# Optimization experiments

Measured on AMD Instinct MI355X. Metric: run time of the kernel, lower is better.

The kernel has to match this reference:

```python
import jax, jax.numpy as jnp
import numpy as np

GROUPS = 32
EPS = 1e-5


def group_norm(x, w, b):
    B, C, H, W = x.shape
    xg = x.reshape(B, GROUPS, C // GROUPS, H, W)
    mu = xg.mean(axis=(2, 3, 4), keepdims=True)
    var = xg.var(axis=(2, 3, 4), keepdims=True)
    xn = ((xg - mu) / jnp.sqrt(var + EPS)).reshape(B, C, H, W)
    return xn * w[None, :, None, None] + b[None, :, None, None]


def setup_inputs() -> dict:
    key = jax.random.key(0)
    ks = jax.random.split(key, 4)
    B, C, H, W = 8, 512, 32, 32
    x = jax.random.normal(ks[0], (B, C, H, W), dtype=jnp.float32)
    gn_w = jnp.ones((C,), dtype=jnp.float32)
    gn_b = jnp.zeros((C,), dtype=jnp.float32)
    # 1x1 conv weights, scaled like typical init for numerical sanity
    qkv_w = jax.random.normal(ks[1], (3 * C, C), dtype=jnp.float32) * (1.0 / np.sqrt(C))
    proj_w = jax.random.normal(ks[2], (C, C), dtype=jnp.float32) * (1.0 / np.sqrt(C))
    proj_b = jnp.zeros((C,), dtype=jnp.float32)
    return {"x": x, "gn_w": gn_w, "gn_b": gn_b, "qkv_w": qkv_w,
            "proj_w": proj_w, "proj_b": proj_b, "num_heads": 8}


def reference(x, gn_w, gn_b, qkv_w, proj_w, proj_b, num_heads):
    B, C, H, W = x.shape
    N = H * W
    head_dim = C // num_heads
    xn = group_norm(x, gn_w, gn_b)
    # 1x1 conv == channel matmul: (B, 3C, N)
    qkv = jnp.einsum('oc,bcn->bon', qkv_w, xn.reshape(B, C, N))
    # faithful to torch: reshape to (B*nh, 3*hd, N) then chunk into thirds
    qkv = qkv.reshape(B * num_heads, 3 * head_dim, N)
    q, k, v = jnp.split(qkv, 3, axis=1)  # each (B*nh, hd, N)
    scale = 1.0 / np.sqrt(np.sqrt(head_dim))
    attn = jax.nn.softmax(jnp.einsum('bct,bcs->bts', q * scale, k * scale), axis=-1)
    h = jnp.einsum('bts,bcs->bct', attn, v)  # (B*nh, hd, N)
    h = h.reshape(B, C, N)
    out = jnp.einsum('oc,bcn->bon', proj_w, h) + proj_b[None, :, None]
    return out.reshape(B, C, H, W) + x
```

## Files before the change

### kernel.cpp

```cpp
#include <hip/hip_runtime.h>

#define B_ 8
#define C_ 512
#define N_ 1024
#define GROUPS_ 32
#define CPG_ 16
#define NH_ 8
#define HD_ 64

typedef _Float16 half8 __attribute__((ext_vector_type(8)));
typedef float f32x4 __attribute__((ext_vector_type(4)));

__global__ __launch_bounds__(256) void cvt_kernel(const float* __restrict__ in,
                                                  _Float16* __restrict__ out,
                                                  int n) {
  const int i = (blockIdx.x * 256 + threadIdx.x) * 4;
  if (i < n) {
    const float4 v = *reinterpret_cast<const float4*>(&in[i]);
    _Float16 h[4] = {(_Float16)v.x, (_Float16)v.y, (_Float16)v.z, (_Float16)v.w};
    *reinterpret_cast<uint2*>(&out[i]) = *reinterpret_cast<uint2*>(&h[0]);
  }
}

__global__ __launch_bounds__(256) void gn_kernel(const float* __restrict__ x,
                                                 const float* __restrict__ gw,
                                                 const float* __restrict__ gb,
                                                 _Float16* __restrict__ xnT) {
  const int bg = blockIdx.x;
  const int b = bg / GROUPS_, g = bg % GROUPS_;
  const float* xp = x + ((size_t)b * C_ + (size_t)g * CPG_) * N_;
  const int tid = threadIdx.x;
  const int total = CPG_ * N_;

  float s = 0.f, ss = 0.f;
  for (int i = tid * 4; i < total; i += 1024) {
    const float4 v = *reinterpret_cast<const float4*>(xp + i);
    s += v.x + v.y + v.z + v.w;
    ss += v.x * v.x + v.y * v.y + v.z * v.z + v.w * v.w;
  }
#pragma unroll
  for (int off = 32; off > 0; off >>= 1) {
    s += __shfl_down(s, off);
    ss += __shfl_down(ss, off);
  }
  __shared__ float red[8];
  __shared__ float stat[2];
  if ((tid & 63) == 0) { red[tid >> 6] = s; red[4 + (tid >> 6)] = ss; }
  __syncthreads();
  if (tid == 0) {
    s = red[0] + red[1] + red[2] + red[3];
    ss = red[4] + red[5] + red[6] + red[7];
    const float inv = 1.0f / (float)total;
    const float mu = s * inv;
    const float var = ss * inv - mu * mu;
    stat[0] = mu;
    stat[1] = rsqrtf(var + 1e-5f);
  }
  __syncthreads();
  __shared__ float wsh[CPG_], bsh[CPG_];
  if (tid < CPG_) {
    const float w = gw[g * CPG_ + tid] * stat[1];
    wsh[tid] = w;
    bsh[tid] = gb[g * CPG_ + tid] - stat[0] * w;
  }
  __syncthreads();
#pragma unroll
  for (int it = 0; it < 4; ++it) {
    const int n = it * 256 + tid;
    _Float16 h[CPG_];
#pragma unroll
    for (int c = 0; c < CPG_; ++c)
      h[c] = (_Float16)(xp[c * N_ + n] * wsh[c] + bsh[c]);
    _Float16* dst = &xnT[((size_t)b * N_ + n) * C_ + g * CPG_];
    *reinterpret_cast<uint4*>(dst) = *reinterpret_cast<uint4*>(&h[0]);
    *reinterpret_cast<uint4*>(dst + 8) = *reinterpret_cast<uint4*>(&h[8]);
  }
}

template <bool OUT_HALF, bool EPI>
__global__ __launch_bounds__(256) void gemm_tn(
    const _Float16* __restrict__ A, long strideAb,
    const _Float16* __restrict__ Bm, long strideBb,
    void* __restrict__ D, long strideDb, int ldd, int K,
    const float* __restrict__ bias, const float* __restrict__ resid,
    long strideRb) {
  const int bc0 = blockIdx.x * 128;
  const int ar0 = blockIdx.y * 128;
  const int b = blockIdx.z;
  const _Float16* Ab = A + (size_t)b * strideAb;
  const _Float16* Bb = Bm + (size_t)b * strideBb;

  __shared__ _Float16 As[128][40];
  __shared__ _Float16 Bs[128][40];

  const int tid = threadIdx.x;
  const int lane = tid & 63;
  const int wid = tid >> 6;
  const int war = (wid >> 1) * 64;
  const int wbc = (wid & 1) * 64;
  const int lg = lane >> 4;
  const int lr = lane & 15;

  const int srow = tid >> 1;
  const int skoff = (tid & 1) * 16;

  f32x4 acc[4][4] = {};

  for (int k0 = 0; k0 < K; k0 += 32) {
    __syncthreads();
    const float4 av0 = *reinterpret_cast<const float4*>(
        &Ab[(size_t)(ar0 + srow) * K + k0 + skoff]);
    const float4 av1 = *reinterpret_cast<const float4*>(
        &Ab[(size_t)(ar0 + srow) * K + k0 + skoff + 8]);
    const float4 bv0 = *reinterpret_cast<const float4*>(
        &Bb[(size_t)(bc0 + srow) * K + k0 + skoff]);
    const float4 bv1 = *reinterpret_cast<const float4*>(
        &Bb[(size_t)(bc0 + srow) * K + k0 + skoff + 8]);
    *reinterpret_cast<float4*>(&As[srow][skoff]) = av0;
    *reinterpret_cast<float4*>(&As[srow][skoff + 8]) = av1;
    *reinterpret_cast<float4*>(&Bs[srow][skoff]) = bv0;
    *reinterpret_cast<float4*>(&Bs[srow][skoff + 8]) = bv1;
    __syncthreads();

    half8 af[4], bf[4];
#pragma unroll
    for (int i = 0; i < 4; ++i)
      af[i] = *reinterpret_cast<const half8*>(&As[war + i * 16 + lr][lg * 8]);
#pragma unroll
    for (int j = 0; j < 4; ++j)
      bf[j] = *reinterpret_cast<const half8*>(&Bs[wbc + j * 16 + lr][lg * 8]);
#pragma unroll
    for (int i = 0; i < 4; ++i)
#pragma unroll
      for (int j = 0; j < 4; ++j)
        acc[i][j] = __builtin_amdgcn_mfma_f32_16x16x32_f16(af[i], bf[j],
                                                           acc[i][j], 0, 0, 0);
  }

  if (OUT_HALF) {
    _Float16* Dp = (_Float16*)D + (size_t)b * strideDb;
#pragma unroll
    for (int i = 0; i < 4; ++i)
#pragma unroll
      for (int r = 0; r < 4; ++r) {
        const int row = ar0 + war + i * 16 + lg * 4 + r;
#pragma unroll
        for (int j = 0; j < 4; ++j) {
          const int col = bc0 + wbc + j * 16 + lr;
          Dp[(size_t)row * ldd + col] = (_Float16)acc[i][j][r];
        }
      }
  }
  if (EPI) {
    float* Dp = (float*)D + (size_t)b * strideDb;
    const float* Rp = resid + (size_t)b * strideRb;
#pragma unroll
    for (int i = 0; i < 4; ++i)
#pragma unroll
      for (int r = 0; r < 4; ++r) {
        const int row = ar0 + war + i * 16 + lg * 4 + r;
        const float bv = bias[row];
#pragma unroll
        for (int j = 0; j < 4; ++j) {
          const int col = bc0 + wbc + j * 16 + lr;
          const size_t off = (size_t)row * ldd + col;
          Dp[off] = acc[i][j][r] + bv + Rp[off];
        }
      }
  }
}

__global__ __launch_bounds__(256) void attn_mfma(const _Float16* __restrict__ qkvT,
                                                 _Float16* __restrict__ hT) {
  const int qt = blockIdx.x;
  const int bh = blockIdx.y;
  const int b = bh >> 3, head = bh & 7;
  const int qb = qt * 64;
  const size_t base = (size_t)b * N_ * 1536 + head * 192;

  __shared__ _Float16 Qs[64][72];
  __shared__ _Float16 Ks[64][72];
  __shared__ _Float16 Vs[64][72];
  __shared__ _Float16 Ps[64][72];

  const int tid = threadIdx.x;
  const int lane = tid & 63;
  const int wid = tid >> 6;
  const int lg = lane >> 4, lr = lane & 15;
  const int tw = wid * 16;
  const int ss = tid >> 2;
  const int sc = (tid & 3) * 16;

  {
    const _Float16* qp = &qkvT[base + (size_t)(qb + ss) * 1536 + sc];
    *reinterpret_cast<float4*>(&Qs[ss][sc]) =
        *reinterpret_cast<const float4*>(qp);
    *reinterpret_cast<float4*>(&Qs[ss][sc + 8]) =
        *reinterpret_cast<const float4*>(qp + 8);
  }

  f32x4 oacc[4] = {};
  float m_run[4], l_run[4];
#pragma unroll
  for (int r = 0; r < 4; ++r) { m_run[r] = -1e30f; l_run[r] = 0.f; }

  for (int sb = 0; sb < N_; sb += 64) {
    __syncthreads();
    {
      const _Float16* kp = &qkvT[base + 64 + (size_t)(sb + ss) * 1536 + sc];
      *reinterpret_cast<float4*>(&Ks[ss][sc]) =
          *reinterpret_cast<const float4*>(kp);
      *reinterpret_cast<float4*>(&Ks[ss][sc + 8]) =
          *reinterpret_cast<const float4*>(kp + 8);
      const _Float16* vp = &qkvT[base + 128 + (size_t)(sb + ss) * 1536 + sc];
      const float4 v0 = *reinterpret_cast<const float4*>(vp);
      const float4 v1 = *reinterpret_cast<const float4*>(vp + 8);
      const _Float16* vh0 = reinterpret_cast<const _Float16*>(&v0);
      const _Float16* vh1 = reinterpret_cast<const _Float16*>(&v1);
#pragma unroll
      for (int ii = 0; ii < 8; ++ii) Vs[sc + ii][ss] = vh0[ii];
#pragma unroll
      for (int ii = 0; ii < 8; ++ii) Vs[sc + 8 + ii][ss] = vh1[ii];
    }
    __syncthreads();

    const half8 qa0 = *reinterpret_cast<const half8*>(&Qs[tw + lr][lg * 8]);
    const half8 qa1 = *reinterpret_cast<const half8*>(&Qs[tw + lr][32 + lg * 8]);
    f32x4 sacc[4] = {};
#pragma unroll
    for (int j = 0; j < 4; ++j) {
      const half8 kb0 = *reinterpret_cast<const half8*>(&Ks[j * 16 + lr][lg * 8]);
      const half8 kb1 =
          *reinterpret_cast<const half8*>(&Ks[j * 16 + lr][32 + lg * 8]);
      sacc[j] = __builtin_amdgcn_mfma_f32_16x16x32_f16(qa0, kb0, sacc[j], 0, 0, 0);
      sacc[j] = __builtin_amdgcn_mfma_f32_16x16x32_f16(qa1, kb1, sacc[j], 0, 0, 0);
    }

#pragma unroll
    for (int r = 0; r < 4; ++r) {
      float mt = -1e30f;
#pragma unroll
      for (int j = 0; j < 4; ++j) {
        sacc[j][r] *= 0.125f;
        mt = fmaxf(mt, sacc[j][r]);
      }
      mt = fmaxf(mt, __shfl_xor(mt, 1));
      mt = fmaxf(mt, __shfl_xor(mt, 2));
      mt = fmaxf(mt, __shfl_xor(mt, 4));
      mt = fmaxf(mt, __shfl_xor(mt, 8));
      const float mn = fmaxf(m_run[r], mt);
      const float alpha = __expf(m_run[r] - mn);
      m_run[r] = mn;
      float ps = 0.f;
#pragma unroll
      for (int j = 0; j < 4; ++j) {
        const float p = __expf(sacc[j][r] - mn);
        sacc[j][r] = p;
        ps += p;
      }
      ps += __shfl_xor(ps, 1);
      ps += __shfl_xor(ps, 2);
      ps += __shfl_xor(ps, 4);
      ps += __shfl_xor(ps, 8);
      l_run[r] = l_run[r] * alpha + ps;
#pragma unroll
      for (int j = 0; j < 4; ++j) {
        oacc[j][r] *= alpha;
        Ps[tw + lg * 4 + r][j * 16 + lr] = (_Float16)sacc[j][r];
      }
    }

    const half8 pa0 = *reinterpret_cast<const half8*>(&Ps[tw + lr][lg * 8]);
    const half8 pa1 = *reinterpret_cast<const half8*>(&Ps[tw + lr][32 + lg * 8]);
#pragma unroll
    for (int j = 0; j < 4; ++j) {
      const half8 vb0 = *reinterpret_cast<const half8*>(&Vs[j * 16 + lr][lg * 8]);
      const half8 vb1 =
          *reinterpret_cast<const half8*>(&Vs[j * 16 + lr][32 + lg * 8]);
      oacc[j] = __builtin_amdgcn_mfma_f32_16x16x32_f16(pa0, vb0, oacc[j], 0, 0, 0);
      oacc[j] = __builtin_amdgcn_mfma_f32_16x16x32_f16(pa1, vb1, oacc[j], 0, 0, 0);
    }
  }

  const size_t hbase = (size_t)b * N_ * C_ + head * HD_;
#pragma unroll
  for (int r = 0; r < 4; ++r) {
    const float inv = 1.f / l_run[r];
    const int t = tw + lg * 4 + r;
#pragma unroll
    for (int j = 0; j < 4; ++j)
      hT[hbase + (size_t)(qb + t) * C_ + j * 16 + lr] =
          (_Float16)(oacc[j][r] * inv);
  }
}

extern "C" void kernel_launch(void* const* d_in, const int* in_sizes, int n_in,
                              void* d_out, int out_size, void* d_ws,
                              size_t ws_size, hipStream_t stream) {
  const float* x = (const float*)d_in[0];
  const float* gn_w = (const float*)d_in[1];
  const float* gn_b = (const float*)d_in[2];
  const float* qkv_w = (const float*)d_in[3];
  const float* proj_w = (const float*)d_in[4];
  const float* proj_b = (const float*)d_in[5];
  float* out = (float*)d_out;

  char* ws = (char*)d_ws;
  _Float16* qw_h = (_Float16*)ws;
  _Float16* pw_h = (_Float16*)(ws + (size_t)1572864);
  _Float16* xnT = (_Float16*)(ws + (size_t)2 * 1024 * 1024);
  _Float16* qkvT = (_Float16*)(ws + (size_t)10 * 1024 * 1024);
  _Float16* hT = (_Float16*)(ws + (size_t)34 * 1024 * 1024);

  cvt_kernel<<<dim3(768), 256, 0, stream>>>(qkv_w, qw_h, 3 * C_ * C_);
  cvt_kernel<<<dim3(256), 256, 0, stream>>>(proj_w, pw_h, C_ * C_);
  gn_kernel<<<dim3(B_ * GROUPS_), 256, 0, stream>>>(x, gn_w, gn_b, xnT);
  gemm_tn<true, false><<<dim3(12, 8, B_), 256, 0, stream>>>(
      xnT, (long)N_ * C_, qw_h, 0L, qkvT, (long)N_ * 3 * C_, 3 * C_, C_,
      nullptr, nullptr, 0L);
  attn_mfma<<<dim3(N_ / 64, B_ * NH_), 256, 0, stream>>>(qkvT, hT);
  gemm_tn<false, true><<<dim3(8, 4, B_), 256, 0, stream>>>(
      pw_h, 0L, hT, (long)N_ * C_, out, (long)C_ * N_, N_, C_,
      proj_b, x, (long)C_ * N_);
}
```

Measured before the change: 209.2 us.

## Restructure attention with 32x32 MFMA, register Q, prefetch, and V-transposed GEMM

Weights are packed into separate QK and V matrices, with the Q rows pre-scaled by the softmax scale times log2(e). V is then produced by its own GEMM directly in transposed layout, which removes the scattered LDS transpose inside attention. Group norm is split into a stats kernel and a normalize kernel that transposes through shared memory for coalesced stores. Attention now uses 32x32x16 MFMA with 256 queries per block and Q held in registers, and it prefetches the next K/V tile into registers. Softmax uses exp2 and skips the rescale unless the max grows past a threshold, and P is kept in registers via lane shuffles instead of LDS. The risks are higher register pressure, lower occupancy with 256 blocks, and fp16 overflow from the lazy rescale.

```diff
diff --git a/kernel.cpp b/kernel.cpp
--- a/kernel.cpp
+++ b/kernel.cpp
@@ -9,23 +9,47 @@
 #define HD_ 64
 
 typedef _Float16 half8 __attribute__((ext_vector_type(8)));
+typedef _Float16 half2v __attribute__((ext_vector_type(2)));
 typedef float f32x4 __attribute__((ext_vector_type(4)));
-
-__global__ __launch_bounds__(256) void cvt_kernel(const float* __restrict__ in,
-                                                  _Float16* __restrict__ out,
-                                                  int n) {
-  const int i = (blockIdx.x * 256 + threadIdx.x) * 4;
-  if (i < n) {
-    const float4 v = *reinterpret_cast<const float4*>(&in[i]);
-    _Float16 h[4] = {(_Float16)v.x, (_Float16)v.y, (_Float16)v.z, (_Float16)v.w};
-    *reinterpret_cast<uint2*>(&out[i]) = *reinterpret_cast<uint2*>(&h[0]);
-  }
-}
-
-__global__ __launch_bounds__(256) void gn_kernel(const float* __restrict__ x,
-                                                 const float* __restrict__ gw,
-                                                 const float* __restrict__ gb,
-                                                 _Float16* __restrict__ xnT) {
+typedef float f32x16 __attribute__((ext_vector_type(16)));
+
+#define QSCALE 0.18033688011112042f
+#define THR_LOG2 11.0f
+
+__global__ __launch_bounds__(256) void pack_weights(
+    const float* __restrict__ qkv_w, const float* __restrict__ proj_w,
+    _Float16* __restrict__ qkw, _Float16* __restrict__ vw,
+    _Float16* __restrict__ pw) {
+  const int R = blockIdx.x * 4 + (threadIdx.x >> 6);
+  const int k = (threadIdx.x & 63) * 8;
+  const float* src;
+  _Float16* dst;
+  float sc = 1.f;
+  if (R < 1024) {
+    const int head = R >> 7, r = R & 127;
+    src = qkv_w + (size_t)(head * 192 + r) * 512;
+    if (r < 64) sc = QSCALE;
+    dst = qkw + (size_t)R * 512;
+  } else if (R < 1536) {
+    const int vr = R - 1024;
+    const int head = vr >> 6, c = vr & 63;
+    src = qkv_w + (size_t)(head * 192 + 128 + c) * 512;
+    dst = vw + (size_t)vr * 512;
+  } else {
+    src = proj_w + (size_t)(R - 1536) * 512;
+    dst = pw + (size_t)(R - 1536) * 512;
+  }
+  const float4 v0 = *reinterpret_cast<const float4*>(src + k);
+  const float4 v1 = *reinterpret_cast<const float4*>(src + k + 4);
+  _Float16 h[8] = {(_Float16)(v0.x * sc), (_Float16)(v0.y * sc),
+                   (_Float16)(v0.z * sc), (_Float16)(v0.w * sc),
+                   (_Float16)(v1.x * sc), (_Float16)(v1.y * sc),
+                   (_Float16)(v1.z * sc), (_Float16)(v1.w * sc)};
+  *reinterpret_cast<float4*>(dst + k) = *reinterpret_cast<float4*>(h);
+}
+
+__global__ __launch_bounds__(256) void gn_stats(const float* __restrict__ x,
+                                                float2* __restrict__ stats) {
   const int bg = blockIdx.x;
   const int b = bg / GROUPS_, g = bg % GROUPS_;
   const float* xp = x + ((size_t)b * C_ + (size_t)g * CPG_) * N_;
@@ -44,7 +68,6 @@
     ss += __shfl_down(ss, off);
   }
   __shared__ float red[8];
-  __shared__ float stat[2];
   if ((tid & 63) == 0) { red[tid >> 6] = s; red[4 + (tid >> 6)] = ss; }
   __syncthreads();
   if (tid == 0) {
@@ -53,28 +76,46 @@
     const float inv = 1.0f / (float)total;
     const float mu = s * inv;
     const float var = ss * inv - mu * mu;
-    stat[0] = mu;
-    stat[1] = rsqrtf(var + 1e-5f);
+    stats[bg] = make_float2(mu, rsqrtf(var + 1e-5f));
+  }
+}
+
+__global__ __launch_bounds__(256) void gn_norm(const float* __restrict__ x,
+                                               const float* __restrict__ gw,
+                                               const float* __restrict__ gb,
+                                               const float2* __restrict__ stats,
+                                               _Float16* __restrict__ xnT) {
+  const int n0 = blockIdx.x * 16;
+  const int b = blockIdx.y;
+  __shared__ _Float16 T[16][520];
+  __shared__ float wsh[512], bsh[512];
+  const int tid = threadIdx.x;
+  for (int c = tid; c < 512; c += 256) {
+    const float2 st = stats[b * 32 + (c >> 4)];
+    const float wv = gw[c] * st.y;
+    wsh[c] = wv;
+    bsh[c] = gb[c] - st.x * wv;
   }
   __syncthreads();
-  __shared__ float wsh[CPG_], bsh[CPG_];
-  if (tid < CPG_) {
-    const float w = gw[g * CPG_ + tid] * stat[1];
-    wsh[tid] = w;
-    bsh[tid] = gb[g * CPG_ + tid] - stat[0] * w;
+  {
+    const int n = tid & 15;
+    const int cb = tid >> 4;
+    const float* xb = x + (size_t)b * C_ * N_ + n0 + n;
+#pragma unroll
+    for (int i = 0; i < 32; ++i) {
+      const int c = i * 16 + cb;
+      T[n][c] = (_Float16)(xb[(size_t)c * N_] * wsh[c] + bsh[c]);
+    }
   }
   __syncthreads();
-#pragma unroll
-  for (int it = 0; it < 4; ++it) {
-    const int n = it * 256 + tid;
-    _Float16 h[CPG_];
-#pragma unroll
-    for (int c = 0; c < CPG_; ++c)
-      h[c] = (_Float16)(xp[c * N_ + n] * wsh[c] + bsh[c]);
-    _Float16* dst = &xnT[((size_t)b * N_ + n) * C_ + g * CPG_];
-    *reinterpret_cast<uint4*>(dst) = *reinterpret_cast<uint4*>(&h[0]);
-    *reinterpret_cast<uint4*>(dst + 8) = *reinterpret_cast<uint4*>(&h[8]);
-  }
+  const int row = tid >> 4;
+  const int seg = tid & 15;
+  _Float16* dst = &xnT[((size_t)b * N_ + n0 + row) * C_ + seg * 32];
+  const _Float16* srcp = &T[row][seg * 32];
+  *reinterpret_cast<float4*>(dst) = *reinterpret_cast<const float4*>(srcp);
+  *reinterpret_cast<float4*>(dst + 8) = *reinterpret_cast<const float4*>(srcp + 8);
+  *reinterpret_cast<float4*>(dst + 16) = *reinterpret_cast<const float4*>(srcp + 16);
+  *reinterpret_cast<float4*>(dst + 24) = *reinterpret_cast<const float4*>(srcp + 24);
 }
 
 template <bool OUT_HALF, bool EPI>
@@ -170,127 +211,176 @@
   }
 }
 
-__global__ __launch_bounds__(256) void attn_mfma(const _Float16* __restrict__ qkvT,
-                                                 _Float16* __restrict__ hT) {
-  const int qt = blockIdx.x;
+__global__ __launch_bounds__(256, 1) void attn_mfma(
+    const _Float16* __restrict__ qkT, const _Float16* __restrict__ vT,
+    _Float16* __restrict__ hT) {
+  const int qb = blockIdx.x * 256;
   const int bh = blockIdx.y;
   const int b = bh >> 3, head = bh & 7;
-  const int qb = qt * 64;
-  const size_t base = (size_t)b * N_ * 1536 + head * 192;
-
-  __shared__ _Float16 Qs[64][72];
+  const int tid = threadIdx.x;
+  const int lane = tid & 63;
+  const int w = tid >> 6;
+  const int l31 = lane & 31;
+  const int lg2 = lane >> 5;
+
   __shared__ _Float16 Ks[64][72];
   __shared__ _Float16 Vs[64][72];
-  __shared__ _Float16 Ps[64][72];
-
-  const int tid = threadIdx.x;
-  const int lane = tid & 63;
-  const int wid = tid >> 6;
-  const int lg = lane >> 4, lr = lane & 15;
-  const int tw = wid * 16;
-  const int ss = tid >> 2;
+
+  const size_t qkbase = (size_t)b * N_ * 1024;
+
+  half8 bfq[2][4];
+#pragma unroll
+  for (int jt = 0; jt < 2; ++jt)
+#pragma unroll
+    for (int kc = 0; kc < 4; ++kc)
+      bfq[jt][kc] = *reinterpret_cast<const half8*>(
+          &qkT[qkbase + (size_t)(qb + w * 64 + jt * 32 + l31) * 1024 +
+               head * 128 + kc * 16 + lg2 * 8]);
+
+  const int sr = tid >> 2;
   const int sc = (tid & 3) * 16;
-
-  {
-    const _Float16* qp = &qkvT[base + (size_t)(qb + ss) * 1536 + sc];
-    *reinterpret_cast<float4*>(&Qs[ss][sc]) =
-        *reinterpret_cast<const float4*>(qp);
-    *reinterpret_cast<float4*>(&Qs[ss][sc + 8]) =
-        *reinterpret_cast<const float4*>(qp + 8);
-  }
-
-  f32x4 oacc[4] = {};
-  float m_run[4], l_run[4];
-#pragma unroll
-  for (int r = 0; r < 4; ++r) { m_run[r] = -1e30f; l_run[r] = 0.f; }
-
-  for (int sb = 0; sb < N_; sb += 64) {
+  const _Float16* kp0 = qkT + qkbase + (size_t)sr * 1024 + head * 128 + 64 + sc;
+  const _Float16* vp0 = vT + ((size_t)bh * 64 + sr) * 1024 + sc;
+
+  float4 kreg0 = *reinterpret_cast<const float4*>(kp0);
+  float4 kreg1 = *reinterpret_cast<const float4*>(kp0 + 8);
+  float4 vreg0 = *reinterpret_cast<const float4*>(vp0);
+  float4 vreg1 = *reinterpret_cast<const float4*>(vp0 + 8);
+
+  f32x16 oacc[2][2];
+#pragma unroll
+  for (int jt = 0; jt < 2; ++jt)
+#pragma unroll
+    for (int ct = 0; ct < 2; ++ct)
+#pragma unroll
+      for (int r = 0; r < 16; ++r) oacc[jt][ct][r] = 0.f;
+  float m_run[2] = {-1e30f, -1e30f};
+  float l_run[2] = {0.f, 0.f};
+
+  for (int t = 0; t < 16; ++t) {
+    __syncthreads();
+    *reinterpret_cast<float4*>(&Ks[sr][sc]) = kreg0;
+    *reinterpret_cast<float4*>(&Ks[sr][sc + 8]) = kreg1;
+    *reinterpret_cast<float4*>(&Vs[sr][sc]) = vreg0;
+    *reinterpret_cast<float4*>(&Vs[sr][sc + 8]) = vreg1;
     __syncthreads();
     {
-      const _Float16* kp = &qkvT[base + 64 + (size_t)(sb + ss) * 1536 + sc];
-      *reinterpret_cast<float4*>(&Ks[ss][sc]) =
-          *reinterpret_cast<const float4*>(kp);
-      *reinterpret_cast<float4*>(&Ks[ss][sc + 8]) =
-          *reinterpret_cast<const float4*>(kp + 8);
-      const _Float16* vp = &qkvT[base + 128 + (size_t)(sb + ss) * 1536 + sc];
-      const float4 v0 = *reinterpret_cast<const float4*>(vp);
-      const float4 v1 = *reinterpret_cast<const float4*>(vp + 8);
-      const _Float16* vh0 = reinterpret_cast<const _Float16*>(&v0);
-      const _Float16* vh1 = reinterpret_cast<const _Float16*>(&v1);
-#pragma unroll
-      for (int ii = 0; ii < 8; ++ii) Vs[sc + ii][ss] = vh0[ii];
-#pragma unroll
-      for (int ii = 0; ii < 8; ++ii) Vs[sc + 8 + ii][ss] = vh1[ii];
+      const int sbn = (t < 15) ? (t + 1) * 64 : 960;
+      kreg0 = *reinterpret_cast<const float4*>(kp0 + (size_t)sbn * 1024);
+      kreg1 = *reinterpret_cast<const float4*>(kp0 + (size_t)sbn * 1024 + 8);
+      vreg0 = *reinterpret_cast<const float4*>(vp0 + sbn);
+      vreg1 = *reinterpret_cast<const float4*>(vp0 + sbn + 8);
     }
-    __syncthreads();
-
-    const half8 qa0 = *reinterpret_cast<const half8*>(&Qs[tw + lr][lg * 8]);
-    const half8 qa1 = *reinterpret_cast<const half8*>(&Qs[tw + lr][32 + lg * 8]);
-    f32x4 sacc[4] = {};
-#pragma unroll
-    for (int j = 0; j < 4; ++j) {
-      const half8 kb0 = *reinterpret_cast<const half8*>(&Ks[j * 16 + lr][lg * 8]);
-      const half8 kb1 =
-          *reinterpret_cast<const half8*>(&Ks[j * 16 + lr][32 + lg * 8]);
-      sacc[j] = __builtin_amdgcn_mfma_f32_16x16x32_f16(qa0, kb0, sacc[j], 0, 0, 0);
-      sacc[j] = __builtin_amdgcn_mfma_f32_16x16x32_f16(qa1, kb1, sacc[j], 0, 0, 0);
+
+    f32x16 sacc[2][2];
+#pragma unroll
+    for (int jt = 0; jt < 2; ++jt)
+#pragma unroll
+      for (int st = 0; st < 2; ++st)
+#pragma unroll
+        for (int r = 0; r < 16; ++r) sacc[jt][st][r] = 0.f;
+#pragma unroll
+    for (int st = 0; st < 2; ++st)
+#pragma unroll
+      for (int kc = 0; kc < 4; ++kc) {
+        const half8 af = *reinterpret_cast<const half8*>(
+            &Ks[st * 32 + l31][kc * 16 + lg2 * 8]);
+        sacc[0][st] = __builtin_amdgcn_mfma_f32_32x32x16_f16(
+            af, bfq[0][kc], sacc[0][st], 0, 0, 0);
+        sacc[1][st] = __builtin_amdgcn_mfma_f32_32x32x16_f16(
+            af, bfq[1][kc], sacc[1][st], 0, 0, 0);
+      }
+
+    half8 pa[2][4];
+#pragma unroll
+    for (int jt = 0; jt < 2; ++jt) {
+      float mt = -1e30f;
+#pragma unroll
+      for (int st = 0; st < 2; ++st)
+#pragma unroll
+        for (int r = 0; r < 16; ++r) mt = fmaxf(mt, sacc[jt][st][r]);
+      mt = fmaxf(mt, __shfl_xor(mt, 32));
+      if (!__all(mt <= m_run[jt] + THR_LOG2)) {
+        const float mn = fmaxf(m_run[jt], mt);
+        const float alpha = exp2f(m_run[jt] - mn);
+        m_run[jt] = mn;
+        l_run[jt] *= alpha;
+#pragma unroll
+        for (int r = 0; r < 16; ++r) {
+          const int qrow = (r & 3) + 8 * (r >> 2) + 4 * lg2;
+          const float ar = __shfl(alpha, qrow);
+          oacc[jt][0][r] *= ar;
+          oacc[jt][1][r] *= ar;
+        }
+      }
+      const float mr = m_run[jt];
+      float ps = 0.f;
+#pragma unroll
+      for (int st = 0; st < 2; ++st)
+#pragma unroll
+        for (int r = 0; r < 16; ++r) {
+          const float p = exp2f(sacc[jt][st][r] - mr);
+          sacc[jt][st][r] = p;
+          ps += p;
+        }
+      ps += __shfl_xor(ps, 32);
+      l_run[jt] += ps;
+
+      unsigned int wo[2][8];
+#pragma unroll
+      for (int st = 0; st < 2; ++st)
+#pragma unroll
+        for (int m = 0; m < 8; ++m) {
+          union { half2v h; unsigned int u; } cv;
+          cv.h.x = (_Float16)sacc[jt][st][2 * m];
+          cv.h.y = (_Float16)sacc[jt][st][2 * m + 1];
+          wo[st][m] = cv.u;
+        }
+#pragma unroll
+      for (int kc = 0; kc < 4; ++kc) {
+        const int st = kc >> 1;
+        const int base = 4 * (kc & 1);
+        const unsigned int a0 = wo[st][base], a1 = wo[st][base + 1];
+        const unsigned int a2 = wo[st][base + 2], a3 = wo[st][base + 3];
+        const unsigned int x0 = __shfl_xor(a0, 32);
+        const unsigned int x1 = __shfl_xor(a1, 32);
+        const unsigned int x2 = __shfl_xor(a2, 32);
+        const unsigned int x3 = __shfl_xor(a3, 32);
+        union { unsigned int u[4]; half8 h; } fr;
+        fr.u[0] = lg2 ? x2 : a0;
+        fr.u[1] = lg2 ? x3 : a1;
+        fr.u[2] = lg2 ? a2 : x0;
+        fr.u[3] = lg2 ? a3 : x1;
+        pa[jt][kc] = fr.h;
+      }
     }
 
 #pragma unroll
-    for (int r = 0; r < 4; ++r) {
-      float mt = -1e30f;
-#pragma unroll
-      for (int j = 0; j < 4; ++j) {
-        sacc[j][r] *= 0.125f;
-        mt = fmaxf(mt, sacc[j][r]);
-      }
-      mt = fmaxf(mt, __shfl_xor(mt, 1));
-      mt = fmaxf(mt, __shfl_xor(mt, 2));
-      mt = fmaxf(mt, __shfl_xor(mt, 4));
-      mt = fmaxf(mt, __shfl_xor(mt, 8));
-      const float mn = fmaxf(m_run[r], mt);
-      const float alpha = __expf(m_run[r] - mn);
-      m_run[r] = mn;
-      float ps = 0.f;
-#pragma unroll
-      for (int j = 0; j < 4; ++j) {
-        const float p = __expf(sacc[j][r] - mn);
-        sacc[j][r] = p;
-        ps += p;
-      }
-      ps += __shfl_xor(ps, 1);
-      ps += __shfl_xor(ps, 2);
-      ps += __shfl_xor(ps, 4);
-      ps += __shfl_xor(ps, 8);
-      l_run[r] = l_run[r] * alpha + ps;
-#pragma unroll
-      for (int j = 0; j < 4; ++j) {
-        oacc[j][r] *= alpha;
-        Ps[tw + lg * 4 + r][j * 16 + lr] = (_Float16)sacc[j][r];
-      }
+    for (int ct = 0; ct < 2; ++ct)
+#pragma unroll
+      for (int ks = 0; ks < 4; ++ks) {
+        const half8 vf = *reinterpret_cast<const half8*>(
+            &Vs[ct * 32 + l31][ks * 16 + lg2 * 8]);
+        oacc[0][ct] = __builtin_amdgcn_mfma_f32_32x32x16_f16(
+            pa[0][ks], vf, oacc[0][ct], 0, 0, 0);
+        oacc[1][ct] = __builtin_amdgcn_mfma_f32_32x32x16_f16(
+            pa[1][ks], vf, oacc[1][ct], 0, 0, 0);
+      }
+  }
+
+  const size_t hbase = ((size_t)b * N_ + qb) * C_ + head * 64;
+#pragma unroll
+  for (int jt = 0; jt < 2; ++jt) {
+    const float linv = 1.f / l_run[jt];
+#pragma unroll
+    for (int r = 0; r < 16; ++r) {
+      const int qrow = (r & 3) + 8 * (r >> 2) + 4 * lg2;
+      const float li = __shfl(linv, qrow);
+      const size_t rowoff = hbase + (size_t)(w * 64 + jt * 32 + qrow) * C_;
+#pragma unroll
+      for (int ct = 0; ct < 2; ++ct)
+        hT[rowoff + ct * 32 + l31] = (_Float16)(oacc[jt][ct][r] * li);
     }
-
-    const half8 pa0 = *reinterpret_cast<const half8*>(&Ps[tw + lr][lg * 8]);
-    const half8 pa1 = *reinterpret_cast<const half8*>(&Ps[tw + lr][32 + lg * 8]);
-#pragma unroll
-    for (int j = 0; j < 4; ++j) {
-      const half8 vb0 = *reinterpret_cast<const half8*>(&Vs[j * 16 + lr][lg * 8]);
-      const half8 vb1 =
-          *reinterpret_cast<const half8*>(&Vs[j * 16 + lr][32 + lg * 8]);
-      oacc[j] = __builtin_amdgcn_mfma_f32_16x16x32_f16(pa0, vb0, oacc[j], 0, 0, 0);
-      oacc[j] = __builtin_amdgcn_mfma_f32_16x16x32_f16(pa1, vb1, oacc[j], 0, 0, 0);
-    }
-  }
-
-  const size_t hbase = (size_t)b * N_ * C_ + head * HD_;
-#pragma unroll
-  for (int r = 0; r < 4; ++r) {
-    const float inv = 1.f / l_run[r];
-    const int t = tw + lg * 4 + r;
-#pragma unroll
-    for (int j = 0; j < 4; ++j)
-      hT[hbase + (size_t)(qb + t) * C_ + j * 16 + lr] =
-          (_Float16)(oacc[j][r] * inv);
   }
 }
 
@@ -306,20 +396,27 @@
   float* out = (float*)d_out;
 
   char* ws = (char*)d_ws;
-  _Float16* qw_h = (_Float16*)ws;
-  _Float16* pw_h = (_Float16*)(ws + (size_t)1572864);
-  _Float16* xnT = (_Float16*)(ws + (size_t)2 * 1024 * 1024);
-  _Float16* qkvT = (_Float16*)(ws + (size_t)10 * 1024 * 1024);
-  _Float16* hT = (_Float16*)(ws + (size_t)34 * 1024 * 1024);
-
-  cvt_kernel<<<dim3(768), 256, 0, stream>>>(qkv_w, qw_h, 3 * C_ * C_);
-  cvt_kernel<<<dim3(256), 256, 0, stream>>>(proj_w, pw_h, C_ * C_);
-  gn_kernel<<<dim3(B_ * GROUPS_), 256, 0, stream>>>(x, gn_w, gn_b, xnT);
-  gemm_tn<true, false><<<dim3(12, 8, B_), 256, 0, stream>>>(
-      xnT, (long)N_ * C_, qw_h, 0L, qkvT, (long)N_ * 3 * C_, 3 * C_, C_,
+  const size_t MB = 1024 * 1024;
+  _Float16* qkw = (_Float16*)(ws);
+  _Float16* vw = (_Float16*)(ws + 1 * MB);
+  _Float16* pw = (_Float16*)(ws + 3 * MB / 2);
+  float2* stats = (float2*)(ws + 2 * MB);
+  _Float16* xnT = (_Float16*)(ws + 3 * MB);
+  _Float16* qkT = (_Float16*)(ws + 11 * MB);
+  _Float16* vT = (_Float16*)(ws + 27 * MB);
+  _Float16* hT = (_Float16*)(ws + 35 * MB);
+
+  pack_weights<<<dim3(512), 256, 0, stream>>>(qkv_w, proj_w, qkw, vw, pw);
+  gn_stats<<<dim3(B_ * GROUPS_), 256, 0, stream>>>(x, stats);
+  gn_norm<<<dim3(64, B_), 256, 0, stream>>>(x, gn_w, gn_b, stats, xnT);
+  gemm_tn<true, false><<<dim3(8, 8, B_), 256, 0, stream>>>(
+      xnT, (long)N_ * C_, qkw, 0L, qkT, (long)N_ * 1024, 1024, C_,
       nullptr, nullptr, 0L);
-  attn_mfma<<<dim3(N_ / 64, B_ * NH_), 256, 0, stream>>>(qkvT, hT);
+  gemm_tn<true, false><<<dim3(8, 4, B_), 256, 0, stream>>>(
+      vw, 0L, xnT, (long)N_ * C_, vT, (long)512 * 1024, 1024, C_,
+      nullptr, nullptr, 0L);
+  attn_mfma<<<dim3(N_ / 256, B_ * NH_), 256, 0, stream>>>(qkT, vT, hT);
   gemm_tn<false, true><<<dim3(8, 4, B_), 256, 0, stream>>>(
-      pw_h, 0L, hT, (long)N_ * C_, out, (long)C_ * N_, N_, C_,
+      pw, 0L, hT, (long)N_ * C_, out, (long)C_ * N_, N_, C_,
       proj_b, x, (long)C_ * N_);
 }
```

Result: faster. 193.3 us (-7.6%).
